# Performance work log

Hardware: AMD Instinct MI355X
Metric: run time of the kernel (lower is better)

## Reference

```python
import jax, jax.numpy as jnp
import numpy as np

B, S, D, H = 1, 2048, 2048, 32
HD = D // H  # head_dim = 64
FF = 4 * D
EPS = 1e-5


def _alibi_slopes(n_heads):
    # standard ALiBi slopes for power-of-2 head counts: 2^(-8i/n)
    return np.array([2.0 ** (-8.0 * (i + 1) / n_heads) for i in range(n_heads)], np.float32)


def setup_inputs() -> dict:
    key = jax.random.key(0)
    ks = jax.random.split(key, 16)
    s = 0.02
    x = jax.random.normal(ks[0], (B, S, D), jnp.float32)
    # alibi bias [B, H, 1, S], broadcast over query positions (HF views alibi as (b, h, 1, kv_len))
    slopes = _alibi_slopes(H)
    alibi_np = slopes[:, None, None] * np.arange(S, dtype=np.float32)[None, None, :]
    alibi = jnp.broadcast_to(jnp.asarray(alibi_np), (B, H, 1, S))
    # additive causal mask [1, 1, S, S]
    causal = np.tril(np.ones((S, S), bool))
    attention_mask = jnp.asarray(np.where(causal, 0.0, -1e9).astype(np.float32))[None, None]
    p = lambda k, shp: s * jax.random.normal(k, shp, jnp.float32)
    return {
        "x": x,
        "alibi": alibi,
        "attention_mask": attention_mask,
        "ln1_g": jnp.ones((D,), jnp.float32), "ln1_b": jnp.zeros((D,), jnp.float32),
        "ln2_g": jnp.ones((D,), jnp.float32), "ln2_b": jnp.zeros((D,), jnp.float32),
        "wqkv": p(ks[1], (D, 3 * D)), "bqkv": jnp.zeros((3 * D,), jnp.float32),
        "wo": p(ks[2], (D, D)), "bo": jnp.zeros((D,), jnp.float32),
        "w1": p(ks[3], (D, FF)), "b1": jnp.zeros((FF,), jnp.float32),
        "w2": p(ks[4], (FF, D)), "b2": jnp.zeros((D,), jnp.float32),
    }


def _layernorm(h, g, b):
    m = h.mean(-1, keepdims=True)
    v = ((h - m) ** 2).mean(-1, keepdims=True)
    return (h - m) * jax.lax.rsqrt(v + EPS) * g + b


def reference(x, alibi, attention_mask, ln1_g, ln1_b, ln2_g, ln2_b,
              wqkv, bqkv, wo, bo, w1, b1, w2, b2):
    b, s, d = x.shape
    inv_norm = 1.0 / np.sqrt(HD).astype(np.float32)
    # --- input layernorm ---
    h = _layernorm(x, ln1_g, ln1_b)
    # --- fused QKV ---
    qkv = h @ wqkv + bqkv
    q, k, v = jnp.split(qkv, 3, axis=-1)
    q = q.reshape(b, s, H, HD).transpose(0, 2, 1, 3)  # [b, h, s, hd]
    k = k.reshape(b, s, H, HD).transpose(0, 2, 1, 3)
    v = v.reshape(b, s, H, HD).transpose(0, 2, 1, 3)
    # --- ALiBi-biased attention (HF falcon alibi path) ---
    scores = jnp.einsum("bhqd,bhkd->bhqk", q, k)          # [b, h, s, s]
    logits = (scores + alibi) * inv_norm + attention_mask  # alibi broadcasts over q dim
    probs = jax.nn.softmax(logits, axis=-1)
    ctx = jnp.einsum("bhqk,bhkd->bhqd", probs, v)
    ctx = ctx.transpose(0, 2, 1, 3).reshape(b, s, d)
    attn_out = ctx @ wo + bo
    # --- residual, post-attn layernorm, MLP (non-parallel falcon-rw layout) ---
    res = x + attn_out
    h2 = _layernorm(res, ln2_g, ln2_b)
    mlp = jax.nn.gelu(h2 @ w1 + b1, approximate=False) @ w2 + b2
    return res + mlp
```

## Files before the change

### kernel.cpp

```cpp
#include <hip/hip_runtime.h>
#include <hip/hip_bf16.h>
#include <cstdint>
#include <cstddef>

static constexpr int Sq  = 2048;
static constexpr int Dm  = 2048;
static constexpr int NH  = 32;
static constexpr int HDm = 64;
static constexpr int FFm = 8192;

typedef __bf16 bf16x8 __attribute__((ext_vector_type(8)));
typedef float  f32x4  __attribute__((ext_vector_type(4)));

__device__ __forceinline__ void async_ld16(const void* g, void* l) {
  __builtin_amdgcn_global_load_lds((const __attribute__((address_space(1))) void*)g,
                                   (__attribute__((address_space(3))) void*)l, 16, 0, 0);
}

#define MFMA16(a, b, c) __builtin_amdgcn_mfma_f32_16x16x32_bf16(a, b, c, 0, 0, 0)

__global__ __launch_bounds__(256)
void tcast_kernel(const float* __restrict__ in, __hip_bfloat16* __restrict__ out,
                  int K, int N) {
  __shared__ float tile[64][65];
  const int tc = blockIdx.x * 64;
  const int tr = blockIdx.y * 64;
  const int cx = threadIdx.x & 63;
  const int ry = threadIdx.x >> 6;
#pragma unroll
  for (int i = 0; i < 16; ++i) {
    int r = ry + i * 4;
    tile[r][cx] = in[(size_t)(tr + r) * N + tc + cx];
  }
  __syncthreads();
#pragma unroll
  for (int i = 0; i < 16; ++i) {
    int r = ry + i * 4;
    out[(size_t)(tc + r) * K + tr + cx] = __float2bfloat16(tile[cx][r]);
  }
}

__global__ __launch_bounds__(256)
void ln_kernel(const float* __restrict__ x, const float* __restrict__ g,
               const float* __restrict__ b, __hip_bfloat16* __restrict__ out) {
  __shared__ float red[4];
  const int t = threadIdx.x;
  const float* xr = x + (size_t)blockIdx.x * Dm;
  float v[8];
  float s = 0.f;
#pragma unroll
  for (int i = 0; i < 8; ++i) { v[i] = xr[t + i * 256]; s += v[i]; }
#pragma unroll
  for (int off = 32; off > 0; off >>= 1) s += __shfl_down(s, off, 64);
  if ((t & 63) == 0) red[t >> 6] = s;
  __syncthreads();
  const float mean = (red[0] + red[1] + red[2] + red[3]) * (1.f / Dm);
  __syncthreads();
  float vs = 0.f;
#pragma unroll
  for (int i = 0; i < 8; ++i) { float d = v[i] - mean; vs += d * d; }
#pragma unroll
  for (int off = 32; off > 0; off >>= 1) vs += __shfl_down(vs, off, 64);
  if ((t & 63) == 0) red[t >> 6] = vs;
  __syncthreads();
  const float inv = rsqrtf((red[0] + red[1] + red[2] + red[3]) * (1.f / Dm) + 1e-5f);
  __hip_bfloat16* orow = out + (size_t)blockIdx.x * Dm;
#pragma unroll
  for (int i = 0; i < 8; ++i) {
    int c = t + i * 256;
    orow[c] = __float2bfloat16((v[i] - mean) * inv * g[c] + b[c]);
  }
}

template <int EPI>
__global__ __launch_bounds__(512)
void gemm256_kernel(const __hip_bfloat16* __restrict__ A,
                    const __hip_bfloat16* __restrict__ Bt,
                    int N, int K,
                    const float* __restrict__ bias,
                    __hip_bfloat16* __restrict__ outb,
                    __hip_bfloat16* __restrict__ qo,
                    __hip_bfloat16* __restrict__ ko,
                    __hip_bfloat16* __restrict__ vo) {
  __shared__ __align__(16) __hip_bfloat16 As[2][256 * 64];
  __shared__ __align__(16) __hip_bfloat16 Bs[2][256 * 64];
  const int t = threadIdx.x;
  const int lane = t & 63, w = t >> 6, quad = lane >> 4, l16 = lane & 15;
  const int wmi = w >> 2, wni = w & 3;
  const int nwg = gridDim.x;
  const int id = blockIdx.x;
  const int xcd = id & 7, q = nwg >> 3, r_ = nwg & 7;
  const int swz = (xcd < r_ ? xcd * (q + 1) : r_ * (q + 1) + (xcd - r_) * q) + (id >> 3);
  const int bm = swz & 7, bn = swz >> 3;
  const __hip_bfloat16* Abase = A + (size_t)bm * 256 * K;
  const __hip_bfloat16* Bbase = Bt + (size_t)bn * 256 * K;
  const int kT = K / 64;

  const int c0 = t, c1 = t + 512;
  const int r0 = c0 >> 3, k0c = (c0 & 7) ^ (r0 & 7);
  const int r1 = c1 >> 3, k1c = (c1 & 7) ^ (r1 & 7);
  const size_t o0 = (size_t)r0 * K + k0c * 8;
  const size_t o1 = (size_t)r1 * K + k1c * 8;
  const size_t halfO = (size_t)128 * K;

  auto stA = [&](int b, int h, int k0) {
    async_ld16(Abase + h * halfO + o0 + k0, &As[b][h * 8192 + c0 * 8]);
    async_ld16(Abase + h * halfO + o1 + k0, &As[b][h * 8192 + c1 * 8]);
  };
  auto stB = [&](int b, int h, int k0) {
    async_ld16(Bbase + h * halfO + o0 + k0, &Bs[b][h * 8192 + c0 * 8]);
    async_ld16(Bbase + h * halfO + o1 + k0, &Bs[b][h * 8192 + c1 * 8]);
  };
  auto ldsA = [&](int b, int r, int ks) {
    return *(const bf16x8*)(&As[b][r * 64 + (((ks * 4 + quad) ^ (r & 7)) << 3)]);
  };
  auto ldsB = [&](int b, int r, int ks) {
    return *(const bf16x8*)(&Bs[b][r * 64 + (((ks * 4 + quad) ^ (r & 7)) << 3)]);
  };

  f32x4 acc[8][4] = {};
  bf16x8 af0[4][2], af1[4][2], bf0[2][2], bf1[2][2];
  const int arow = wmi * 128 + l16;
  const int brow = wni * 64 + l16;

#define BAR() asm volatile("s_barrier" ::: "memory")
#define LGKM0() do { asm volatile("s_waitcnt lgkmcnt(0)" ::: "memory"); \
                     __builtin_amdgcn_sched_barrier(0); } while (0)

  stA(0, 0, 0); stA(0, 1, 0); stB(0, 0, 0); stB(0, 1, 0);
  stA(1, 0, 64); stB(1, 0, 64);
  asm volatile("s_waitcnt vmcnt(4)" ::: "memory");
  BAR();

  for (int tt = 0; tt < kT; ++tt) {
    const int buf = tt & 1;
    const int kn1 = (tt + 1) * 64, kn2 = (tt + 2) * 64;
#pragma unroll
    for (int mt = 0; mt < 4; ++mt) {
      af0[mt][0] = ldsA(buf, arow + mt * 16, 0);
      af0[mt][1] = ldsA(buf, arow + mt * 16, 1);
    }
#pragma unroll
    for (int nt = 0; nt < 2; ++nt) {
      bf0[nt][0] = ldsB(buf, brow + nt * 16, 0);
      bf0[nt][1] = ldsB(buf, brow + nt * 16, 1);
    }
    if (tt + 1 < kT) stA(buf ^ 1, 1, kn1);
    BAR(); LGKM0();
    __builtin_amdgcn_s_setprio(1);
#pragma unroll
    for (int mt = 0; mt < 4; ++mt)
#pragma unroll
      for (int nt = 0; nt < 2; ++nt) {
        acc[mt][nt] = MFMA16(af0[mt][0], bf0[nt][0], acc[mt][nt]);
        acc[mt][nt] = MFMA16(af0[mt][1], bf0[nt][1], acc[mt][nt]);
      }
    __builtin_amdgcn_s_setprio(0);
    BAR();
#pragma unroll
    for (int mt = 0; mt < 4; ++mt) {
      af1[mt][0] = ldsA(buf, arow + 64 + mt * 16, 0);
      af1[mt][1] = ldsA(buf, arow + 64 + mt * 16, 1);
    }
    if (tt + 1 < kT) stB(buf ^ 1, 1, kn1);
    BAR(); LGKM0();
    __builtin_amdgcn_s_setprio(1);
#pragma unroll
    for (int mt = 0; mt < 4; ++mt)
#pragma unroll
      for (int nt = 0; nt < 2; ++nt) {
        acc[4 + mt][nt] = MFMA16(af1[mt][0], bf0[nt][0], acc[4 + mt][nt]);
        acc[4 + mt][nt] = MFMA16(af1[mt][1], bf0[nt][1], acc[4 + mt][nt]);
      }
    __builtin_amdgcn_s_setprio(0);
    BAR();
#pragma unroll
    for (int nt = 0; nt < 2; ++nt) {
      bf1[nt][0] = ldsB(buf, brow + 32 + nt * 16, 0);
      bf1[nt][1] = ldsB(buf, brow + 32 + nt * 16, 1);
    }
    if (tt + 2 < kT) stA(buf, 0, kn2);
    BAR(); LGKM0();
    __builtin_amdgcn_s_setprio(1);
#pragma unroll
    for (int mt = 0; mt < 4; ++mt)
#pragma unroll
      for (int nt = 0; nt < 2; ++nt) {
        acc[mt][2 + nt] = MFMA16(af0[mt][0], bf1[nt][0], acc[mt][2 + nt]);
        acc[mt][2 + nt] = MFMA16(af0[mt][1], bf1[nt][1], acc[mt][2 + nt]);
      }
    __builtin_amdgcn_s_setprio(0);
    BAR();
    if (tt + 2 < kT) stB(buf, 0, kn2);
    BAR();
    __builtin_amdgcn_s_setprio(1);
#pragma unroll
    for (int mt = 0; mt < 4; ++mt)
#pragma unroll
      for (int nt = 0; nt < 2; ++nt) {
        acc[4 + mt][2 + nt] = MFMA16(af1[mt][0], bf1[nt][0], acc[4 + mt][2 + nt]);
        acc[4 + mt][2 + nt] = MFMA16(af1[mt][1], bf1[nt][1], acc[4 + mt][2 + nt]);
      }
    __builtin_amdgcn_s_setprio(0);
    if (tt + 2 < kT) asm volatile("s_waitcnt vmcnt(4)" ::: "memory");
    else             asm volatile("s_waitcnt vmcnt(0)" ::: "memory");
    BAR();
  }
#undef BAR
#undef LGKM0

#pragma unroll
  for (int mf = 0; mf < 8; ++mf) {
#pragma unroll
    for (int nf = 0; nf < 4; ++nf) {
      const int n = bn * 256 + wni * 64 + nf * 16 + l16;
      const float bb = bias[n];
#pragma unroll
      for (int rr = 0; rr < 4; ++rr) {
        const int m = bm * 256 + wmi * 128 + mf * 16 + quad * 4 + rr;
        float val = acc[mf][nf][rr] + bb;
        if constexpr (EPI == 0) {
          int which = n >> 11, d2 = n & 2047;
          int hh = d2 >> 6, hd = d2 & 63;
          if (which == 0)
            qo[((size_t)hh * Sq + m) * HDm + hd] = __float2bfloat16(val * 0.125f);
          else if (which == 1)
            ko[((size_t)hh * Sq + m) * HDm + hd] = __float2bfloat16(val);
          else
            vo[((size_t)hh * HDm + hd) * Sq + m] = __float2bfloat16(val);
        } else {
          float gg = 0.5f * val * (1.0f + erff(val * 0.70710678118654752f));
          outb[(size_t)m * N + n] = __float2bfloat16(gg);
        }
      }
    }
  }
}

template <int EPI>
__global__ __launch_bounds__(256)
void gemm_kernel(const __hip_bfloat16* __restrict__ A,
                 const __hip_bfloat16* __restrict__ Bt,
                 int N, int K, int Ksub,
                 const float* __restrict__ bias,
                 const float* __restrict__ addsrc,
                 float* __restrict__ outf,
                 __hip_bfloat16* __restrict__ outb,
                 __hip_bfloat16* __restrict__ po) {
  __shared__ __align__(16) __hip_bfloat16 As[2][128 * 32];
  __shared__ __align__(16) __hip_bfloat16 Bs[2][128 * 32];
  const int t = threadIdx.x;
  const int lane = t & 63, w = t >> 6, quad = lane >> 4, l16 = lane & 15;
  const int nbx = gridDim.x;
  const int id = blockIdx.y * nbx + blockIdx.x;
  const int chunk = (nbx * 16) >> 3;
  const int nid = (id & 7) * chunk + (id >> 3);
  const int bn = nid >> 4, bm = nid & 15;
  const int bz = blockIdx.z;
  const int wm = (w & 1) * 64, wn = (w >> 1) * 64;
  const __hip_bfloat16* Abase = A + (size_t)bm * 128 * K;
  const __hip_bfloat16* Bbase = Bt + (size_t)bn * 128 * K;
  const int kBeg = bz * Ksub;
  const int kSteps = Ksub / 32;

  const int c0 = t, c1 = t + 256;
  const int r0 = c0 >> 2, g0 = ((c0 & 3) - (r0 >> 1)) & 3;
  const int r1 = c1 >> 2, g1 = ((c1 & 3) - (r1 >> 1)) & 3;
  const __hip_bfloat16* a0p = Abase + (size_t)r0 * K + g0 * 8;
  const __hip_bfloat16* a1p = Abase + (size_t)r1 * K + g1 * 8;
  const __hip_bfloat16* b0p = Bbase + (size_t)r0 * K + g0 * 8;
  const __hip_bfloat16* b1p = Bbase + (size_t)r1 * K + g1 * 8;

  auto stage = [&](int b, int k0) {
    async_ld16(a0p + k0, &As[b][c0 * 8]);
    async_ld16(a1p + k0, &As[b][c1 * 8]);
    async_ld16(b0p + k0, &Bs[b][c0 * 8]);
    async_ld16(b1p + k0, &Bs[b][c1 * 8]);
  };

  f32x4 acc[4][4] = {};
  auto compute = [&](int b) {
    bf16x8 af[4], bfv[4];
#pragma unroll
    for (int i = 0; i < 4; ++i) {
      int row = wm + i * 16 + l16;
      int p = (quad + (row >> 1)) & 3;
      af[i] = *(const bf16x8*)(&As[b][row * 32 + p * 8]);
    }
#pragma unroll
    for (int i = 0; i < 4; ++i) {
      int row = wn + i * 16 + l16;
      int p = (quad + (row >> 1)) & 3;
      bfv[i] = *(const bf16x8*)(&Bs[b][row * 32 + p * 8]);
    }
#pragma unroll
    for (int mt = 0; mt < 4; ++mt)
#pragma unroll
      for (int nt = 0; nt < 4; ++nt)
        acc[mt][nt] = MFMA16(af[mt], bfv[nt], acc[mt][nt]);
  };

#define PIPE_BAR() asm volatile("s_waitcnt vmcnt(0)\n\ts_barrier" ::: "memory")
  stage(0, kBeg);
  PIPE_BAR();
  int buf = 0;
  for (int i = 0; i < kSteps; ++i) {
    if (i + 1 < kSteps) stage(buf ^ 1, kBeg + (i + 1) * 32);
    compute(buf);
    PIPE_BAR();
    buf ^= 1;
  }
#undef PIPE_BAR

#pragma unroll
  for (int mt = 0; mt < 4; ++mt) {
#pragma unroll
    for (int nt = 0; nt < 4; ++nt) {
      const int n = bn * 128 + wn + nt * 16 + l16;
      const float bz2 = bias[n];
#pragma unroll
      for (int r = 0; r < 4; ++r) {
        const int m = bm * 128 + wm + mt * 16 + quad * 4 + r;
        float val = acc[mt][nt][r];
        if constexpr (EPI == 2) {
          val += bz2;
          float gg = 0.5f * val * (1.0f + erff(val * 0.70710678118654752f));
          outb[(size_t)m * N + n] = __float2bfloat16(gg);
        } else {
          if (bz == 0)
            outf[(size_t)m * N + n] = addsrc[(size_t)m * N + n] + bz2 + val;
          else
            po[(size_t)m * N + n] = __float2bfloat16(val);
        }
      }
    }
  }
}

__global__ __launch_bounds__(256)
void addp_kernel(float* __restrict__ out, const __hip_bfloat16* __restrict__ p) {
  const int i = (blockIdx.x * 256 + threadIdx.x) * 4;
  float4 o = *(const float4*)(out + i);
  const __hip_bfloat16* pp = p + i;
  o.x += (float)pp[0]; o.y += (float)pp[1]; o.z += (float)pp[2]; o.w += (float)pp[3];
  *(float4*)(out + i) = o;
}

__global__ __launch_bounds__(256)
void attn_kernel(const __hip_bfloat16* __restrict__ qb,
                 const __hip_bfloat16* __restrict__ kb,
                 const __hip_bfloat16* __restrict__ vt,
                 const float* __restrict__ alibi,
                 __hip_bfloat16* __restrict__ ctx) {
  __shared__ __align__(16) __hip_bfloat16 Kl[2][64 * 64];
  __shared__ __align__(16) __hip_bfloat16 Vl[2][64 * 64];
  __shared__ __align__(16) __hip_bfloat16 Pl[4][16 * 64];
  const int pi = blockIdx.x, h = blockIdx.y;
  const int qA = pi, qB = (Sq / 64 - 1) - pi;
  const int t = threadIdx.x, w = t >> 6, lane = t & 63, quad = lane >> 4, l16 = lane & 15;
  const __hip_bfloat16* qh = qb + (size_t)h * Sq * HDm;
  const __hip_bfloat16* kh = kb + (size_t)h * Sq * HDm;
  const __hip_bfloat16* vh = vt + (size_t)h * HDm * Sq;
  const float* al = alibi + (size_t)h * Sq;

  const int rA = qA * 64 + w * 16 + l16;
  const int rB = qB * 64 + w * 16 + l16;
  const bf16x8 qA0 = *(const bf16x8*)(qh + (size_t)rA * HDm + quad * 8);
  const bf16x8 qA1 = *(const bf16x8*)(qh + (size_t)rA * HDm + 32 + quad * 8);
  const bf16x8 qB0 = *(const bf16x8*)(qh + (size_t)rB * HDm + quad * 8);
  const bf16x8 qB1 = *(const bf16x8*)(qh + (size_t)rB * HDm + 32 + quad * 8);

  auto stageS = [&](int b, int s) {
    const int kbk = (s <= qA) ? s : s - qA - 1;
#pragma unroll
    for (int j = 0; j < 2; ++j) {
      int c = j * 256 + t;
      int row = c >> 3;
      int swz = (c & 7) ^ (row & 7);
      async_ld16(kh + (size_t)(kbk * 64 + row) * HDm + swz * 8, &Kl[b][c * 8]);
      async_ld16(vh + (size_t)row * Sq + kbk * 64 + swz * 8, &Vl[b][c * 8]);
    }
  };

  f32x4 o[4] = {};
  float m_i[4], l_i[4];
#pragma unroll
  for (int r = 0; r < 4; ++r) { m_i[r] = -3e38f; l_i[r] = 0.f; }

  const int total = qA + qB + 2;
  stageS(0, 0);
  int buf = 0;
  for (int s = 0; s < total; ++s, buf ^= 1) {
    __syncthreads();
    if (s + 1 < total) stageS(buf ^ 1, s + 1);
    const bool ph = (s > qA);
    const int kbk = ph ? s - qA - 1 : s;
    const int qblk = ph ? qB : qA;
    const bf16x8 a0 = ph ? qB0 : qA0;
    const bf16x8 a1 = ph ? qB1 : qA1;

    f32x4 sf[4];
    const f32x4 zero = {};
#pragma unroll
    for (int nt = 0; nt < 4; ++nt) {
      int row = nt * 16 + l16;
      bf16x8 kf0 = *(const bf16x8*)(&Kl[buf][row * 64 + ((quad ^ (row & 7)) << 3)]);
      bf16x8 kf1 = *(const bf16x8*)(&Kl[buf][row * 64 + (((4 + quad) ^ (row & 7)) << 3)]);
      sf[nt] = __builtin_amdgcn_mfma_f32_16x16x32_bf16(a0, kf0, zero, 0, 0, 0);
      sf[nt] = __builtin_amdgcn_mfma_f32_16x16x32_bf16(a1, kf1, sf[nt], 0, 0, 0);
    }
    const bool diag = (kbk == qblk);
    float mrow[4] = {-3e38f, -3e38f, -3e38f, -3e38f};
#pragma unroll
    for (int nt = 0; nt < 4; ++nt) {
      const float ab = al[kbk * 64 + nt * 16 + l16] * 0.125f;
      const int kcol = nt * 16 + l16;
#pragma unroll
      for (int r = 0; r < 4; ++r) {
        float vv = sf[nt][r] + ab;
        if (diag && kcol > w * 16 + quad * 4 + r) vv = -3e38f;
        sf[nt][r] = vv;
        mrow[r] = fmaxf(mrow[r], vv);
      }
    }
#pragma unroll
    for (int off = 8; off > 0; off >>= 1)
#pragma unroll
      for (int r = 0; r < 4; ++r)
        mrow[r] = fmaxf(mrow[r], __shfl_xor(mrow[r], off, 64));
    float alpha[4], rs[4], p[4][4];
#pragma unroll
    for (int r = 0; r < 4; ++r) {
      float mn = fmaxf(m_i[r], mrow[r]);
      alpha[r] = __expf(m_i[r] - mn);
      m_i[r] = mn;
    }
#pragma unroll
    for (int nt = 0; nt < 4; ++nt)
#pragma unroll
      for (int r = 0; r < 4; ++r) p[nt][r] = __expf(sf[nt][r] - m_i[r]);
#pragma unroll
    for (int r = 0; r < 4; ++r) rs[r] = p[0][r] + p[1][r] + p[2][r] + p[3][r];
#pragma unroll
    for (int off = 8; off > 0; off >>= 1)
#pragma unroll
      for (int r = 0; r < 4; ++r) rs[r] += __shfl_xor(rs[r], off, 64);
#pragma unroll
    for (int r = 0; r < 4; ++r) l_i[r] = l_i[r] * alpha[r] + rs[r];
#pragma unroll
    for (int dt = 0; dt < 4; ++dt)
#pragma unroll
      for (int r = 0; r < 4; ++r) o[dt][r] *= alpha[r];
    __hip_bfloat16* pw = &Pl[w][0];
#pragma unroll
    for (int nt = 0; nt < 4; ++nt)
#pragma unroll
      for (int r = 0; r < 4; ++r) {
        int prow = quad * 4 + r;
        int e = nt * 16 + l16;
        int c16 = e >> 3;
        pw[prow * 64 + ((c16 ^ (prow & 7)) << 3) + (e & 7)] = __float2bfloat16(p[nt][r]);
      }
    asm volatile("s_waitcnt lgkmcnt(0)" ::: "memory");
    const bf16x8 pa0 = *(const bf16x8*)(pw + l16 * 64 + ((quad ^ (l16 & 7)) << 3));
    const bf16x8 pa1 = *(const bf16x8*)(pw + l16 * 64 + (((4 + quad) ^ (l16 & 7)) << 3));
#pragma unroll
    for (int dt = 0; dt < 4; ++dt) {
      int row = dt * 16 + l16;
      bf16x8 v0 = *(const bf16x8*)(&Vl[buf][row * 64 + ((quad ^ (row & 7)) << 3)]);
      bf16x8 v1 = *(const bf16x8*)(&Vl[buf][row * 64 + (((4 + quad) ^ (row & 7)) << 3)]);
      o[dt] = __builtin_amdgcn_mfma_f32_16x16x32_bf16(pa0, v0, o[dt], 0, 0, 0);
      o[dt] = __builtin_amdgcn_mfma_f32_16x16x32_bf16(pa1, v1, o[dt], 0, 0, 0);
    }
    if (s == qA) {
#pragma unroll
      for (int dt = 0; dt < 4; ++dt)
#pragma unroll
        for (int r = 0; r < 4; ++r) {
          int srow = qA * 64 + w * 16 + quad * 4 + r;
          ctx[(size_t)srow * Dm + h * HDm + dt * 16 + l16] =
              __float2bfloat16(o[dt][r] / l_i[r]);
          o[dt][r] = 0.f;
        }
#pragma unroll
      for (int r = 0; r < 4; ++r) { m_i[r] = -3e38f; l_i[r] = 0.f; }
    }
  }
#pragma unroll
  for (int dt = 0; dt < 4; ++dt)
#pragma unroll
    for (int r = 0; r < 4; ++r) {
      int srow = qB * 64 + w * 16 + quad * 4 + r;
      ctx[(size_t)srow * Dm + h * HDm + dt * 16 + l16] =
          __float2bfloat16(o[dt][r] / l_i[r]);
    }
}

extern "C" void kernel_launch(void* const* d_in, const int* in_sizes, int n_in,
                              void* d_out, int out_size, void* d_ws, size_t ws_size,
                              hipStream_t stream) {
  const float* x     = (const float*)d_in[0];
  const float* alibi = (const float*)d_in[1];
  const float* ln1g  = (const float*)d_in[3];
  const float* ln1b  = (const float*)d_in[4];
  const float* ln2g  = (const float*)d_in[5];
  const float* ln2b  = (const float*)d_in[6];
  const float* wqkv  = (const float*)d_in[7];
  const float* bqkv  = (const float*)d_in[8];
  const float* wo    = (const float*)d_in[9];
  const float* bo    = (const float*)d_in[10];
  const float* w1    = (const float*)d_in[11];
  const float* b1    = (const float*)d_in[12];
  const float* w2    = (const float*)d_in[13];
  const float* b2    = (const float*)d_in[14];
  float* out = (float*)d_out;

  char* p = (char*)d_ws;
  auto alloc = [&](size_t bytes) {
    char* r = p;
    p += (bytes + 255) & ~(size_t)255;
    return r;
  };
  constexpr size_t SD2 = (size_t)Sq * Dm * 2;
  char* R2 = alloc((size_t)FFm * Dm * 2);
  char* R1 = alloc(4 * SD2);
  __hip_bfloat16* hb   = (__hip_bfloat16*)alloc(SD2);
  float*          resb = (float*)alloc((size_t)Sq * Dm * 4);

  __hip_bfloat16* wqkvT = (__hip_bfloat16*)R2;
  __hip_bfloat16* w1T   = (__hip_bfloat16*)R2;
  __hip_bfloat16* w2T   = (__hip_bfloat16*)R2;
  __hip_bfloat16* qbuf  = (__hip_bfloat16*)(R1 + 0 * SD2);
  __hip_bfloat16* kbuf  = (__hip_bfloat16*)(R1 + 1 * SD2);
  __hip_bfloat16* vtbuf = (__hip_bfloat16*)(R1 + 2 * SD2);
  __hip_bfloat16* ctxb  = (__hip_bfloat16*)(R1 + 3 * SD2);
  __hip_bfloat16* woT   = (__hip_bfloat16*)(R1 + 0 * SD2);
  __hip_bfloat16* t1b   = (__hip_bfloat16*)R1;
  __hip_bfloat16* part  = hb;

  tcast_kernel<<<dim3(3 * Dm / 64, Dm / 64), 256, 0, stream>>>(wqkv, wqkvT, Dm, 3 * Dm);
  ln_kernel<<<Sq, 256, 0, stream>>>(x, ln1g, ln1b, hb);
  gemm256_kernel<0><<<dim3((3 * Dm / 256) * (Sq / 256)), 512, 0, stream>>>(
      hb, wqkvT, 3 * Dm, Dm, bqkv, nullptr, qbuf, kbuf, vtbuf);
  tcast_kernel<<<dim3(FFm / 64, Dm / 64), 256, 0, stream>>>(w1, w1T, Dm, FFm);
  attn_kernel<<<dim3(Sq / 128, NH), 256, 0, stream>>>(qbuf, kbuf, vtbuf, alibi, ctxb);
  tcast_kernel<<<dim3(Dm / 64, Dm / 64), 256, 0, stream>>>(wo, woT, Dm, Dm);
  gemm_kernel<3><<<dim3(Dm / 128, Sq / 128, 2), 256, 0, stream>>>(
      ctxb, woT, Dm, Dm, Dm / 2, bo, x, resb, nullptr, part);
  addp_kernel<<<(Sq * Dm) / 1024, 256, 0, stream>>>(resb, part);
  ln_kernel<<<Sq, 256, 0, stream>>>(resb, ln2g, ln2b, hb);
  gemm256_kernel<2><<<dim3((FFm / 256) * (Sq / 256)), 512, 0, stream>>>(
      hb, w1T, FFm, Dm, b1, t1b, nullptr, nullptr, nullptr);
  tcast_kernel<<<dim3(Dm / 64, FFm / 64), 256, 0, stream>>>(w2, w2T, FFm, Dm);
  gemm_kernel<3><<<dim3(Dm / 128, Sq / 128, 2), 256, 0, stream>>>(
      t1b, w2T, Dm, FFm, FFm / 2, b2, resb, out, nullptr, part);
  addp_kernel<<<(Sq * Dm) / 1024, 256, 0, stream>>>(out, part);
}
```

Before: 654.7 us.

## Use 256x256 GEMM with 4-way split-K for output and down projections

Replaces the 128x128 split-K-2 gemm_kernel used for the Wo and W2 projections with the larger 256x256 gemm256 kernel run as a 4-way split-K, with three bf16 partial buffers summed by a new addp3 kernel. The gemm256 prefetch schedule is also reworked to load both halves of the next-next tile together, waiting on vmcnt(8). The aim is higher MFMA efficiency and data reuse from bigger tiles while keeping enough blocks (64 tiles x 4) to fill the GPU. The cost is extra partial-sum traffic, a bigger workspace, and added bf16 rounding of the partials.

```diff
diff --git a/kernel.cpp b/kernel.cpp
--- a/kernel.cpp
+++ b/kernel.cpp
@@ -76,12 +76,15 @@
 __global__ __launch_bounds__(512)
 void gemm256_kernel(const __hip_bfloat16* __restrict__ A,
                     const __hip_bfloat16* __restrict__ Bt,
-                    int N, int K,
+                    int N, int K, int Ksub,
                     const float* __restrict__ bias,
+                    const float* __restrict__ addsrc,
+                    float* __restrict__ outf,
                     __hip_bfloat16* __restrict__ outb,
                     __hip_bfloat16* __restrict__ qo,
                     __hip_bfloat16* __restrict__ ko,
-                    __hip_bfloat16* __restrict__ vo) {
+                    __hip_bfloat16* __restrict__ vo,
+                    __hip_bfloat16* __restrict__ po) {
   __shared__ __align__(16) __hip_bfloat16 As[2][256 * 64];
   __shared__ __align__(16) __hip_bfloat16 Bs[2][256 * 64];
   const int t = threadIdx.x;
@@ -92,9 +95,11 @@
   const int xcd = id & 7, q = nwg >> 3, r_ = nwg & 7;
   const int swz = (xcd < r_ ? xcd * (q + 1) : r_ * (q + 1) + (xcd - r_) * q) + (id >> 3);
   const int bm = swz & 7, bn = swz >> 3;
+  const int bz = blockIdx.z;
   const __hip_bfloat16* Abase = A + (size_t)bm * 256 * K;
   const __hip_bfloat16* Bbase = Bt + (size_t)bn * 256 * K;
-  const int kT = K / 64;
+  const int kBeg = bz * Ksub;
+  const int kT = Ksub / 64;
 
   const int c0 = t, c1 = t + 512;
   const int r0 = c0 >> 3, k0c = (c0 & 7) ^ (r0 & 7);
@@ -127,14 +132,16 @@
 #define LGKM0() do { asm volatile("s_waitcnt lgkmcnt(0)" ::: "memory"); \
                      __builtin_amdgcn_sched_barrier(0); } while (0)
 
-  stA(0, 0, 0); stA(0, 1, 0); stB(0, 0, 0); stB(0, 1, 0);
-  stA(1, 0, 64); stB(1, 0, 64);
-  asm volatile("s_waitcnt vmcnt(4)" ::: "memory");
+  stA(0, 0, kBeg); stA(0, 1, kBeg); stB(0, 0, kBeg); stB(0, 1, kBeg);
+  stA(1, 0, kBeg + 64); stA(1, 1, kBeg + 64);
+  stB(1, 0, kBeg + 64); stB(1, 1, kBeg + 64);
+  asm volatile("s_waitcnt vmcnt(8)" ::: "memory");
   BAR();
 
   for (int tt = 0; tt < kT; ++tt) {
     const int buf = tt & 1;
-    const int kn1 = (tt + 1) * 64, kn2 = (tt + 2) * 64;
+    const int kn2 = kBeg + (tt + 2) * 64;
+    const bool pre = (tt + 2 < kT);
 #pragma unroll
     for (int mt = 0; mt < 4; ++mt) {
       af0[mt][0] = ldsA(buf, arow + mt * 16, 0);
@@ -145,7 +152,6 @@
       bf0[nt][0] = ldsB(buf, brow + nt * 16, 0);
       bf0[nt][1] = ldsB(buf, brow + nt * 16, 1);
     }
-    if (tt + 1 < kT) stA(buf ^ 1, 1, kn1);
     BAR(); LGKM0();
     __builtin_amdgcn_s_setprio(1);
 #pragma unroll
@@ -162,7 +168,6 @@
       af1[mt][0] = ldsA(buf, arow + 64 + mt * 16, 0);
       af1[mt][1] = ldsA(buf, arow + 64 + mt * 16, 1);
     }
-    if (tt + 1 < kT) stB(buf ^ 1, 1, kn1);
     BAR(); LGKM0();
     __builtin_amdgcn_s_setprio(1);
 #pragma unroll
@@ -179,7 +184,7 @@
       bf1[nt][0] = ldsB(buf, brow + 32 + nt * 16, 0);
       bf1[nt][1] = ldsB(buf, brow + 32 + nt * 16, 1);
     }
-    if (tt + 2 < kT) stA(buf, 0, kn2);
+    if (pre) { stA(buf, 0, kn2); stA(buf, 1, kn2); }
     BAR(); LGKM0();
     __builtin_amdgcn_s_setprio(1);
 #pragma unroll
@@ -191,7 +196,7 @@
       }
     __builtin_amdgcn_s_setprio(0);
     BAR();
-    if (tt + 2 < kT) stB(buf, 0, kn2);
+    if (pre) { stB(buf, 0, kn2); stB(buf, 1, kn2); }
     BAR();
     __builtin_amdgcn_s_setprio(1);
 #pragma unroll
@@ -202,8 +207,8 @@
         acc[4 + mt][2 + nt] = MFMA16(af1[mt][1], bf1[nt][1], acc[4 + mt][2 + nt]);
       }
     __builtin_amdgcn_s_setprio(0);
-    if (tt + 2 < kT) asm volatile("s_waitcnt vmcnt(4)" ::: "memory");
-    else             asm volatile("s_waitcnt vmcnt(0)" ::: "memory");
+    if (pre) asm volatile("s_waitcnt vmcnt(8)" ::: "memory");
+    else     asm volatile("s_waitcnt vmcnt(0)" ::: "memory");
     BAR();
   }
 #undef BAR
@@ -218,8 +223,9 @@
 #pragma unroll
       for (int rr = 0; rr < 4; ++rr) {
         const int m = bm * 256 + wmi * 128 + mf * 16 + quad * 4 + rr;
-        float val = acc[mf][nf][rr] + bb;
+        float val = acc[mf][nf][rr];
         if constexpr (EPI == 0) {
+          val += bb;
           int which = n >> 11, d2 = n & 2047;
           int hh = d2 >> 6, hd = d2 & 63;
           if (which == 0)
@@ -228,109 +234,15 @@
             ko[((size_t)hh * Sq + m) * HDm + hd] = __float2bfloat16(val);
           else
             vo[((size_t)hh * HDm + hd) * Sq + m] = __float2bfloat16(val);
-        } else {
-          float gg = 0.5f * val * (1.0f + erff(val * 0.70710678118654752f));
-          outb[(size_t)m * N + n] = __float2bfloat16(gg);
-        }
-      }
-    }
-  }
-}
-
-template <int EPI>
-__global__ __launch_bounds__(256)
-void gemm_kernel(const __hip_bfloat16* __restrict__ A,
-                 const __hip_bfloat16* __restrict__ Bt,
-                 int N, int K, int Ksub,
-                 const float* __restrict__ bias,
-                 const float* __restrict__ addsrc,
-                 float* __restrict__ outf,
-                 __hip_bfloat16* __restrict__ outb,
-                 __hip_bfloat16* __restrict__ po) {
-  __shared__ __align__(16) __hip_bfloat16 As[2][128 * 32];
-  __shared__ __align__(16) __hip_bfloat16 Bs[2][128 * 32];
-  const int t = threadIdx.x;
-  const int lane = t & 63, w = t >> 6, quad = lane >> 4, l16 = lane & 15;
-  const int nbx = gridDim.x;
-  const int id = blockIdx.y * nbx + blockIdx.x;
-  const int chunk = (nbx * 16) >> 3;
-  const int nid = (id & 7) * chunk + (id >> 3);
-  const int bn = nid >> 4, bm = nid & 15;
-  const int bz = blockIdx.z;
-  const int wm = (w & 1) * 64, wn = (w >> 1) * 64;
-  const __hip_bfloat16* Abase = A + (size_t)bm * 128 * K;
-  const __hip_bfloat16* Bbase = Bt + (size_t)bn * 128 * K;
-  const int kBeg = bz * Ksub;
-  const int kSteps = Ksub / 32;
-
-  const int c0 = t, c1 = t + 256;
-  const int r0 = c0 >> 2, g0 = ((c0 & 3) - (r0 >> 1)) & 3;
-  const int r1 = c1 >> 2, g1 = ((c1 & 3) - (r1 >> 1)) & 3;
-  const __hip_bfloat16* a0p = Abase + (size_t)r0 * K + g0 * 8;
-  const __hip_bfloat16* a1p = Abase + (size_t)r1 * K + g1 * 8;
-  const __hip_bfloat16* b0p = Bbase + (size_t)r0 * K + g0 * 8;
-  const __hip_bfloat16* b1p = Bbase + (size_t)r1 * K + g1 * 8;
-
-  auto stage = [&](int b, int k0) {
-    async_ld16(a0p + k0, &As[b][c0 * 8]);
-    async_ld16(a1p + k0, &As[b][c1 * 8]);
-    async_ld16(b0p + k0, &Bs[b][c0 * 8]);
-    async_ld16(b1p + k0, &Bs[b][c1 * 8]);
-  };
-
-  f32x4 acc[4][4] = {};
-  auto compute = [&](int b) {
-    bf16x8 af[4], bfv[4];
-#pragma unroll
-    for (int i = 0; i < 4; ++i) {
-      int row = wm + i * 16 + l16;
-      int p = (quad + (row >> 1)) & 3;
-      af[i] = *(const bf16x8*)(&As[b][row * 32 + p * 8]);
-    }
-#pragma unroll
-    for (int i = 0; i < 4; ++i) {
-      int row = wn + i * 16 + l16;
-      int p = (quad + (row >> 1)) & 3;
-      bfv[i] = *(const bf16x8*)(&Bs[b][row * 32 + p * 8]);
-    }
-#pragma unroll
-    for (int mt = 0; mt < 4; ++mt)
-#pragma unroll
-      for (int nt = 0; nt < 4; ++nt)
-        acc[mt][nt] = MFMA16(af[mt], bfv[nt], acc[mt][nt]);
-  };
-
-#define PIPE_BAR() asm volatile("s_waitcnt vmcnt(0)\n\ts_barrier" ::: "memory")
-  stage(0, kBeg);
-  PIPE_BAR();
-  int buf = 0;
-  for (int i = 0; i < kSteps; ++i) {
-    if (i + 1 < kSteps) stage(buf ^ 1, kBeg + (i + 1) * 32);
-    compute(buf);
-    PIPE_BAR();
-    buf ^= 1;
-  }
-#undef PIPE_BAR
-
-#pragma unroll
-  for (int mt = 0; mt < 4; ++mt) {
-#pragma unroll
-    for (int nt = 0; nt < 4; ++nt) {
-      const int n = bn * 128 + wn + nt * 16 + l16;
-      const float bz2 = bias[n];
-#pragma unroll
-      for (int r = 0; r < 4; ++r) {
-        const int m = bm * 128 + wm + mt * 16 + quad * 4 + r;
-        float val = acc[mt][nt][r];
-        if constexpr (EPI == 2) {
-          val += bz2;
+        } else if constexpr (EPI == 2) {
+          val += bb;
           float gg = 0.5f * val * (1.0f + erff(val * 0.70710678118654752f));
           outb[(size_t)m * N + n] = __float2bfloat16(gg);
         } else {
           if (bz == 0)
-            outf[(size_t)m * N + n] = addsrc[(size_t)m * N + n] + bz2 + val;
+            outf[(size_t)m * N + n] = addsrc[(size_t)m * N + n] + bb + val;
           else
-            po[(size_t)m * N + n] = __float2bfloat16(val);
+            po[(size_t)(bz - 1) * Sq * N + (size_t)m * N + n] = __float2bfloat16(val);
         }
       }
     }
@@ -338,11 +250,15 @@
 }
 
 __global__ __launch_bounds__(256)
-void addp_kernel(float* __restrict__ out, const __hip_bfloat16* __restrict__ p) {
-  const int i = (blockIdx.x * 256 + threadIdx.x) * 4;
+void addp3_kernel(float* __restrict__ out, const __hip_bfloat16* __restrict__ p) {
+  const size_t i = ((size_t)blockIdx.x * 256 + threadIdx.x) * 4;
+  const size_t st = (size_t)Sq * Dm;
   float4 o = *(const float4*)(out + i);
-  const __hip_bfloat16* pp = p + i;
-  o.x += (float)pp[0]; o.y += (float)pp[1]; o.z += (float)pp[2]; o.w += (float)pp[3];
+#pragma unroll
+  for (int s = 0; s < 3; ++s) {
+    const __hip_bfloat16* pp = p + s * st + i;
+    o.x += (float)pp[0]; o.y += (float)pp[1]; o.z += (float)pp[2]; o.w += (float)pp[3];
+  }
   *(float4*)(out + i) = o;
 }
 
@@ -524,8 +440,9 @@
   constexpr size_t SD2 = (size_t)Sq * Dm * 2;
   char* R2 = alloc((size_t)FFm * Dm * 2);
   char* R1 = alloc(4 * SD2);
-  __hip_bfloat16* hb   = (__hip_bfloat16*)alloc(SD2);
-  float*          resb = (float*)alloc((size_t)Sq * Dm * 4);
+  __hip_bfloat16* hb    = (__hip_bfloat16*)alloc(SD2);
+  float*          resb  = (float*)alloc((size_t)Sq * Dm * 4);
+  __hip_bfloat16* part3 = (__hip_bfloat16*)alloc(3 * SD2);
 
   __hip_bfloat16* wqkvT = (__hip_bfloat16*)R2;
   __hip_bfloat16* w1T   = (__hip_bfloat16*)R2;
@@ -536,23 +453,22 @@
   __hip_bfloat16* ctxb  = (__hip_bfloat16*)(R1 + 3 * SD2);
   __hip_bfloat16* woT   = (__hip_bfloat16*)(R1 + 0 * SD2);
   __hip_bfloat16* t1b   = (__hip_bfloat16*)R1;
-  __hip_bfloat16* part  = hb;
 
   tcast_kernel<<<dim3(3 * Dm / 64, Dm / 64), 256, 0, stream>>>(wqkv, wqkvT, Dm, 3 * Dm);
   ln_kernel<<<Sq, 256, 0, stream>>>(x, ln1g, ln1b, hb);
   gemm256_kernel<0><<<dim3((3 * Dm / 256) * (Sq / 256)), 512, 0, stream>>>(
-      hb, wqkvT, 3 * Dm, Dm, bqkv, nullptr, qbuf, kbuf, vtbuf);
+      hb, wqkvT, 3 * Dm, Dm, Dm, bqkv, nullptr, nullptr, nullptr, qbuf, kbuf, vtbuf, nullptr);
   tcast_kernel<<<dim3(FFm / 64, Dm / 64), 256, 0, stream>>>(w1, w1T, Dm, FFm);
   attn_kernel<<<dim3(Sq / 128, NH), 256, 0, stream>>>(qbuf, kbuf, vtbuf, alibi, ctxb);
   tcast_kernel<<<dim3(Dm / 64, Dm / 64), 256, 0, stream>>>(wo, woT, Dm, Dm);
-  gemm_kernel<3><<<dim3(Dm / 128, Sq / 128, 2), 256, 0, stream>>>(
-      ctxb, woT, Dm, Dm, Dm / 2, bo, x, resb, nullptr, part);
-  addp_kernel<<<(Sq * Dm) / 1024, 256, 0, stream>>>(resb, part);
+  gemm256_kernel<3><<<dim3((Dm / 256) * (Sq / 256), 1, 4), 512, 0, stream>>>(
+      ctxb, woT, Dm, Dm, Dm / 4, bo, x, resb, nullptr, nullptr, nullptr, nullptr, part3);
+  addp3_kernel<<<(Sq * Dm) / 1024, 256, 0, stream>>>(resb, part3);
   ln_kernel<<<Sq, 256, 0, stream>>>(resb, ln2g, ln2b, hb);
   gemm256_kernel<2><<<dim3((FFm / 256) * (Sq / 256)), 512, 0, stream>>>(
-      hb, w1T, FFm, Dm, b1, t1b, nullptr, nullptr, nullptr);
+      hb, w1T, FFm, Dm, Dm, b1, nullptr, nullptr, t1b, nullptr, nullptr, nullptr, nullptr);
   tcast_kernel<<<dim3(Dm / 64, FFm / 64), 256, 0, stream>>>(w2, w2T, FFm, Dm);
-  gemm_kernel<3><<<dim3(Dm / 128, Sq / 128, 2), 256, 0, stream>>>(
-      t1b, w2T, Dm, FFm, FFm / 2, b2, resb, out, nullptr, part);
-  addp_kernel<<<(Sq * Dm) / 1024, 256, 0, stream>>>(out, part);
-}
+  gemm256_kernel<3><<<dim3((Dm / 256) * (Sq / 256), 1, 4), 512, 0, stream>>>(
+      t1b, w2T, Dm, FFm, FFm / 4, b2, resb, out, nullptr, nullptr, nullptr, nullptr, part3);
+  addp3_kernel<<<(Sq * Dm) / 1024, 256, 0, stream>>>(out, part3);
+}
```

Result: slower. 690.4 us (+5.5%).
